# Optimization experiments

Measured on AMD Instinct MI355X. Metric: run time of the kernel, lower is better.

The kernel has to match this reference:

```python
import jax, jax.numpy as jnp
import numpy as np

ALPHA = 0.25
GAMMA = 2.0
HUBER_DELTA = 0.5  # init kwarg delta
REG_BETA = 1.0 / 9.0


def calc_iou(a, b):
    # a: [A,4] anchors, b: [M,4] gt boxes, xyxy
    area = (b[:, 2] - b[:, 0]) * (b[:, 3] - b[:, 1])  # [M]
    iw = jnp.clip(jnp.minimum(a[:, 2:3], b[:, 2]) - jnp.maximum(a[:, 0:1], b[:, 0]), 0.0)
    ih = jnp.clip(jnp.minimum(a[:, 3:4], b[:, 3]) - jnp.maximum(a[:, 1:2], b[:, 1]), 0.0)
    ua = jnp.clip(((a[:, 2] - a[:, 0]) * (a[:, 3] - a[:, 1]))[:, None] + area - iw * ih, 1e-8)
    return iw * ih / ua  # [A,M]


def _per_sample(cls, reg, dist, ann, anchor):
    # cls [A,C], reg [A,4], dist [A,1], ann [M,6], anchor [A,4]
    aw = anchor[:, 2] - anchor[:, 0]
    ah = anchor[:, 3] - anchor[:, 1]
    acx = anchor[:, 0] + 0.5 * aw
    acy = anchor[:, 1] + 0.5 * ah

    valid = ann[:, 4] != -1.0  # padding annotations have class == -1
    cls = jnp.clip(cls, 1e-4, 1.0 - 1e-4)

    iou = jnp.where(valid[None, :], calc_iou(anchor, ann[:, :4]), -1.0)  # [A,M]
    iou_max = iou.max(axis=1)
    iou_arg = iou.argmax(axis=1)
    assigned = ann[iou_arg]  # [A,6]

    pos = iou_max >= 0.5
    num_pos = pos.sum()
    denom = jnp.maximum(num_pos.astype(cls.dtype), 1.0)

    labels = assigned[:, 4].astype(jnp.int32)
    onehot = jax.nn.one_hot(labels, cls.shape[1], dtype=cls.dtype)
    # -1 = ignore, 0 = negative (IoU<0.4 or positive-but-not-this-class), 1 = assigned class
    targets = jnp.where(pos[:, None], onehot,
                        jnp.where((iou_max < 0.4)[:, None], 0.0, -1.0))

    af = jnp.where(targets == 1.0, ALPHA, 1.0 - ALPHA)
    fw = af * jnp.where(targets == 1.0, 1.0 - cls, cls) ** GAMMA
    bce = -(targets * jnp.log(cls) + (1.0 - targets) * jnp.log(1.0 - cls))
    cls_loss = jnp.where(targets != -1.0, fw * bce, 0.0).sum() / denom

    # empty-annotation fallback: all anchors treated as background
    cls_loss_empty = ((1.0 - ALPHA) * cls ** GAMMA * (-jnp.log(1.0 - cls))).sum()
    has_ann = valid.any()
    cls_loss = jnp.where(has_ann, cls_loss, cls_loss_empty)

    gw_raw = assigned[:, 2] - assigned[:, 0]
    gh_raw = assigned[:, 3] - assigned[:, 1]
    gcx = assigned[:, 0] + 0.5 * gw_raw  # centers use unclamped w/h (as in torch code)
    gcy = assigned[:, 1] + 0.5 * gh_raw
    gw = jnp.clip(gw_raw, 1.0)
    gh = jnp.clip(gh_raw, 1.0)
    t = jnp.stack([(gcx - acx) / aw, (gcy - acy) / ah,
                   jnp.log(gw / aw), jnp.log(gh / ah)], axis=1)
    t = t / jnp.asarray([0.1, 0.1, 0.2, 0.2], dtype=cls.dtype)
    diff = jnp.abs(t - reg)
    rl = jnp.where(diff <= REG_BETA, 0.5 * 9.0 * diff ** 2, diff - 0.5 / 9.0)
    posf = pos.astype(cls.dtype)
    reg_loss = jnp.where(num_pos > 0, (rl * posf[:, None]).sum() / (denom * 4.0), 0.0)

    # --- distance Huber loss (delta=0.5), positives only ---
    d = jnp.abs(dist[:, 0] - assigned[:, 5])
    hl = jnp.where(d <= HUBER_DELTA, 0.5 * d ** 2, HUBER_DELTA * (d - 0.5 * HUBER_DELTA))
    dist_loss = jnp.where(num_pos > 0, (hl * posf).sum() / denom, 0.0)

    return cls_loss, reg_loss, dist_loss


def reference(classifications, regressions, distances, anchors, annotations):
    anchor = anchors[0]
    cl, rl, dl = jax.vmap(_per_sample, in_axes=(0, 0, 0, 0, None))(
        classifications, regressions, distances, annotations, anchor)
    return (jnp.mean(cl, keepdims=True),
            jnp.mean(rl, keepdims=True),
            jnp.mean(dl, keepdims=True))


def setup_inputs() -> dict:
    key = jax.random.key(0)
    ks = jax.random.split(key, 10)
    B, A, C, M = 8, 120000, 80, 32
    IMG = 800.0

    classifications = jax.random.uniform(ks[0], (B, A, C), dtype=jnp.float32)
    regressions = jax.random.normal(ks[1], (B, A, 4), dtype=jnp.float32)
    distances = jax.random.normal(ks[2], (B, A, 1), dtype=jnp.float32) * 10.0 + 50.0

    # anchors: valid xyxy boxes over an 800px image
    acx = jax.random.uniform(ks[3], (A,), minval=0.0, maxval=IMG)
    acy = jax.random.uniform(ks[4], (A,), minval=0.0, maxval=IMG)
    aw = jax.random.uniform(ks[5], (A, 2), minval=16.0, maxval=256.0)
    anchors = jnp.stack([acx - 0.5 * aw[:, 0], acy - 0.5 * aw[:, 1],
                         acx + 0.5 * aw[:, 0], acy + 0.5 * aw[:, 1]], axis=1)[None].astype(jnp.float32)

    # annotations: [B,M,6] = x1,y1,x2,y2,class,distance (all valid)
    gc = jax.random.uniform(ks[6], (B, M, 2), minval=100.0, maxval=IMG - 100.0)
    gs = jax.random.uniform(ks[7], (B, M, 2), minval=32.0, maxval=300.0)
    boxes = jnp.concatenate([gc - 0.5 * gs, gc + 0.5 * gs], axis=-1)
    labels = jax.random.randint(ks[8], (B, M, 1), 0, C).astype(jnp.float32)
    gdist = jax.random.uniform(ks[9], (B, M, 1), minval=1.0, maxval=100.0)
    annotations = jnp.concatenate([boxes, labels, gdist], axis=-1).astype(jnp.float32)

    return {"classifications": classifications, "regressions": regressions,
            "distances": distances, "anchors": anchors, "annotations": annotations}
```

## Files before the change

### kernel.cpp

```cpp
#include <hip/hip_runtime.h>
#include <hip/hip_bf16.h>


typedef float v4f __attribute__((ext_vector_type(4)));

#define LN2_075 0.51986038542f

__device__ __forceinline__ float wave_reduce_sum(float v) {
#pragma unroll
    for (int off = 32; off > 0; off >>= 1) v += __shfl_down(v, off);
    return v;
}

__device__ __forceinline__ float smooth_l1(float d) {
    return d <= (1.0f / 9.0f) ? 4.5f * d * d : d - (0.5f / 9.0f);
}

__device__ __forceinline__ float proc4(v4f cv, float acc) {
#pragma unroll
    for (int j = 0; j < 4; ++j) {
        const float c = fminf(fmaxf(cv[j], 1e-4f), 1.0f - 1e-4f);
        acc = fmaf(c * c, __log2f(1.0f - c), acc);
    }
    return acc;
}

template <int CPA>
__global__ __launch_bounds__(256) void main_kernel(
    const float* __restrict__ cls, const float* __restrict__ reg,
    const float* __restrict__ dist, const float* __restrict__ anchors,
    const float* __restrict__ ann, float* __restrict__ partA,
    float4* __restrict__ partB, int A, int M, int SBLK, int nb) {
    const int b = blockIdx.y;
    const int tid = threadIdx.x;
    const int lane = tid & 63;
    const int wid = tid >> 6;

    if (blockIdx.x < SBLK) {
        const int NC4 = A * CPA;
        const v4f* __restrict__ p = (const v4f*)(cls + (size_t)b * NC4 * 4);
        const int s = SBLK << 8;
        int i = (blockIdx.x << 8) + tid;
        float acc = 0.f;
        for (; i + 3 * s < NC4; i += 4 * s) {
            const v4f a0 = p[i];
            const v4f a1 = p[i + s];
            const v4f a2 = p[i + 2 * s];
            const v4f a3 = p[i + 3 * s];
            acc = proc4(a0, acc);
            acc = proc4(a1, acc);
            acc = proc4(a2, acc);
            acc = proc4(a3, acc);
        }
        for (; i < NC4; i += s) acc = proc4(p[i], acc);

        __shared__ float s_red[4];
        acc = wave_reduce_sum(acc);
        if (lane == 0) s_red[wid] = acc;
        __syncthreads();
        if (tid == 0)
            partA[(size_t)b * SBLK + blockIdx.x] = s_red[0] + s_red[1] + s_red[2] + s_red[3];
        return;
    }

    const int blk = blockIdx.x - SBLK;
    const int base = blk << 8;

    __shared__ float s_ann[64 * 6];
    const float* annb = ann + (size_t)b * M * 6;
    for (int i = tid; i < M * 6; i += 256) s_ann[i] = annb[i];
    __syncthreads();

    const int a = base + tid;
    float l_npos = 0.f, l_reg = 0.f, l_dist = 0.f;
    int st = -1;
    if (a < A) {
        const float4 av = *(const float4*)(anchors + (size_t)a * 4);
        const float aw = av.z - av.x, ah = av.w - av.y;
        const float acx = av.x + 0.5f * aw, acy = av.y + 0.5f * ah;
        const float aarea = aw * ah;

        float best = -1.0f;
        int bi = 0;
        for (int m = 0; m < M; ++m) {
            const float* g = s_ann + m * 6;
            float iou = -1.0f;
            if (g[4] != -1.0f) {
                float iw = fmaxf(fminf(av.z, g[2]) - fmaxf(av.x, g[0]), 0.f);
                float ih = fmaxf(fminf(av.w, g[3]) - fmaxf(av.y, g[1]), 0.f);
                float inter = iw * ih;
                float area = (g[2] - g[0]) * (g[3] - g[1]);
                float ua = fmaxf(aarea + area - inter, 1e-8f);
                iou = inter / ua;
            }
            if (iou > best) { best = iou; bi = m; }
        }

        if (best >= 0.5f) {
            const float* g = s_ann + bi * 6;
            st = (int)g[4];
            l_npos = 1.f;
            const float4 rv = *(const float4*)(reg + ((size_t)b * A + a) * 4);
            const float gwr = g[2] - g[0], ghr = g[3] - g[1];
            const float gcx = g[0] + 0.5f * gwr, gcy = g[1] + 0.5f * ghr;
            const float gw = fmaxf(gwr, 1.f), gh = fmaxf(ghr, 1.f);
            const float t0 = ((gcx - acx) / aw) / 0.1f;
            const float t1 = ((gcy - acy) / ah) / 0.1f;
            const float t2 = __logf(gw / aw) / 0.2f;
            const float t3 = __logf(gh / ah) / 0.2f;
            l_reg = smooth_l1(fabsf(t0 - rv.x)) + smooth_l1(fabsf(t1 - rv.y)) +
                    smooth_l1(fabsf(t2 - rv.z)) + smooth_l1(fabsf(t3 - rv.w));
            const float dv = dist[(size_t)b * A + a];
            const float dd = fabsf(dv - g[5]);
            l_dist = dd <= 0.5f ? 0.5f * dd * dd : 0.5f * (dd - 0.25f);
        } else if (best >= 0.4f) {
            st = -2;
        }
    }

    const v4f* __restrict__ clsb = (const v4f*)(cls + ((size_t)b * A + base) * (CPA * 4));
    float corr = 0.f;
    if (st >= 0) {
        const float cr = cls[((size_t)b * A + a) * (CPA * 4) + st];
        const float c = fminf(fmaxf(cr, 1e-4f), 1.0f - 1e-4f);
        const float om = 1.0f - c;
        corr = LN2_075 * (c * c * __log2f(om))
               + 0.25f * om * om * (-__logf(c));
    } else if (st == -2) {
        float part = 0.f;
#pragma unroll
        for (int k = 0; k < CPA; ++k) part = proc4(clsb[(size_t)tid * CPA + k], part);
        corr = LN2_075 * part;
    }

    __shared__ float s_red4[4][4];
    const float w0 = wave_reduce_sum(l_npos);
    const float w1 = wave_reduce_sum(corr);
    const float w2 = wave_reduce_sum(l_reg);
    const float w3 = wave_reduce_sum(l_dist);
    if (lane == 0) {
        s_red4[0][wid] = w0; s_red4[1][wid] = w1; s_red4[2][wid] = w2; s_red4[3][wid] = w3;
    }
    __syncthreads();
    if (tid == 0) {
        float4 p;
        p.x = s_red4[0][0] + s_red4[0][1] + s_red4[0][2] + s_red4[0][3];
        p.y = s_red4[1][0] + s_red4[1][1] + s_red4[1][2] + s_red4[1][3];
        p.z = s_red4[2][0] + s_red4[2][1] + s_red4[2][2] + s_red4[2][3];
        p.w = s_red4[3][0] + s_red4[3][1] + s_red4[3][2] + s_red4[3][3];
        partB[(size_t)b * nb + blk] = p;
    }
}

__global__ void finalize_kernel(const float* __restrict__ partA,
                                const float4* __restrict__ partB,
                                float* __restrict__ out, int B, int SBLK, int nb) {
    const int lane = threadIdx.x & 63;
    const int b = threadIdx.x >> 6;
    __shared__ float s_res[8][3];
    if (b < B) {
        float sa = 0.f, np_ = 0.f, corr = 0.f, rs = 0.f, ds = 0.f;
        for (int i = lane; i < SBLK; i += 64) sa += partA[(size_t)b * SBLK + i];
        for (int i = lane; i < nb; i += 64) {
            const float4 p = partB[(size_t)b * nb + i];
            np_ += p.x; corr += p.y; rs += p.z; ds += p.w;
        }
        sa = wave_reduce_sum(sa);
        np_ = wave_reduce_sum(np_);
        corr = wave_reduce_sum(corr);
        rs = wave_reduce_sum(rs);
        ds = wave_reduce_sum(ds);
        if (lane == 0) {
            const float cls_total = fmaf(sa, -LN2_075, corr);
            const float denom = fmaxf(np_, 1.f);
            s_res[b][0] = cls_total / denom;
            s_res[b][1] = np_ > 0.f ? rs / (denom * 4.f) : 0.f;
            s_res[b][2] = np_ > 0.f ? ds / denom : 0.f;
        }
    }
    __syncthreads();
    if (threadIdx.x == 0) {
        float c = 0.f, r = 0.f, d = 0.f;
        for (int i = 0; i < B; ++i) { c += s_res[i][0]; r += s_res[i][1]; d += s_res[i][2]; }
        out[0] = c / (float)B;
        out[1] = r / (float)B;
        out[2] = d / (float)B;
    }
}

__global__ __launch_bounds__(256) void fused_generic_kernel(
    const float* __restrict__ cls, const float* __restrict__ reg,
    const float* __restrict__ dist, const float* __restrict__ anchors,
    const float* __restrict__ ann, float4* __restrict__ partials,
    int A, int C, int M, int nb) {
    const int b = blockIdx.y;
    const int base = blockIdx.x << 8;
    const int tid = threadIdx.x;
    const int cpa = C >> 2;

    __shared__ float s_ann[64 * 6];
    __shared__ signed char s_state[256];
    const float* annb = ann + (size_t)b * M * 6;
    for (int i = tid; i < M * 6; i += 256) s_ann[i] = annb[i];
    s_state[tid] = -2;
    __syncthreads();

    const int a = base + tid;
    float l_npos = 0.f, l_reg = 0.f, l_dist = 0.f;
    if (a < A) {
        const float4 av = *(const float4*)(anchors + (size_t)a * 4);
        const float aw = av.z - av.x, ah = av.w - av.y;
        const float acx = av.x + 0.5f * aw, acy = av.y + 0.5f * ah;
        const float aarea = aw * ah;
        float best = -1.0f;
        int bi = 0;
        for (int m = 0; m < M; ++m) {
            const float* g = s_ann + m * 6;
            float iou = -1.0f;
            if (g[4] != -1.0f) {
                float iw = fmaxf(fminf(av.z, g[2]) - fmaxf(av.x, g[0]), 0.f);
                float ih = fmaxf(fminf(av.w, g[3]) - fmaxf(av.y, g[1]), 0.f);
                float inter = iw * ih;
                float area = (g[2] - g[0]) * (g[3] - g[1]);
                float ua = fmaxf(aarea + area - inter, 1e-8f);
                iou = inter / ua;
            }
            if (iou > best) { best = iou; bi = m; }
        }
        signed char st;
        if (best >= 0.5f) {
            const float* g = s_ann + bi * 6;
            st = (signed char)(int)g[4];
            l_npos = 1.f;
            const float4 rv = *(const float4*)(reg + ((size_t)b * A + a) * 4);
            const float gwr = g[2] - g[0], ghr = g[3] - g[1];
            const float gcx = g[0] + 0.5f * gwr, gcy = g[1] + 0.5f * ghr;
            const float gw = fmaxf(gwr, 1.f), gh = fmaxf(ghr, 1.f);
            const float t0 = ((gcx - acx) / aw) / 0.1f;
            const float t1 = ((gcy - acy) / ah) / 0.1f;
            const float t2 = __logf(gw / aw) / 0.2f;
            const float t3 = __logf(gh / ah) / 0.2f;
            l_reg = smooth_l1(fabsf(t0 - rv.x)) + smooth_l1(fabsf(t1 - rv.y)) +
                    smooth_l1(fabsf(t2 - rv.z)) + smooth_l1(fabsf(t3 - rv.w));
            const float dv = dist[(size_t)b * A + a];
            const float dd = fabsf(dv - g[5]);
            l_dist = dd <= 0.5f ? 0.5f * dd * dd : 0.5f * (dd - 0.25f);
        } else if (best < 0.4f) {
            st = -1;
        } else {
            st = -2;
        }
        s_state[tid] = st;
    }
    __syncthreads();

    const float4* __restrict__ clsb = (const float4*)(cls + ((size_t)b * A + base) * C);
    int a_local = tid / cpa;
    int cc = tid % cpa;
    const int dA = 256 / cpa;
    const int dC = 256 % cpa;
    float lsum = 0.f;
    for (int k = 0; k < cpa; ++k) {
        const int st = s_state[a_local];
        if (st != -2) {
            const float4 cv = clsb[k * 256 + tid];
            const int c0 = cc << 2;
#pragma unroll
            for (int j = 0; j < 4; ++j) {
                float c = j == 0 ? cv.x : j == 1 ? cv.y : j == 2 ? cv.z : cv.w;
                c = fminf(fmaxf(c, 1e-4f), 1.0f - 1e-4f);
                const bool ispos = (st == c0 + j);
                const float om = 1.0f - c;
                const float x = ispos ? c : om;
                const float w = ispos ? 0.25f * om * om : 0.75f * c * c;
                lsum -= w * __logf(x);
            }
        }
        a_local += dA;
        cc += dC;
        if (cc >= cpa) { cc -= cpa; ++a_local; }
    }

    __shared__ float s_red[4][4];
    const float w0 = wave_reduce_sum(l_npos);
    const float w1 = wave_reduce_sum(lsum);
    const float w2 = wave_reduce_sum(l_reg);
    const float w3 = wave_reduce_sum(l_dist);
    const int lane = tid & 63, wid = tid >> 6;
    if (lane == 0) {
        s_red[0][wid] = w0; s_red[1][wid] = w1; s_red[2][wid] = w2; s_red[3][wid] = w3;
    }
    __syncthreads();
    if (tid == 0) {
        float4 p;
        p.x = s_red[0][0] + s_red[0][1] + s_red[0][2] + s_red[0][3];
        p.y = s_red[1][0] + s_red[1][1] + s_red[1][2] + s_red[1][3];
        p.z = s_red[2][0] + s_red[2][1] + s_red[2][2] + s_red[2][3];
        p.w = s_red[3][0] + s_red[3][1] + s_red[3][2] + s_red[3][3];
        partials[(size_t)b * nb + blockIdx.x] = p;
    }
}

extern "C" void kernel_launch(void* const* d_in, const int* in_sizes, int n_in,
                              void* d_out, int out_size, void* d_ws, size_t ws_size,
                              hipStream_t stream) {
    const float* cls     = (const float*)d_in[0];
    const float* reg     = (const float*)d_in[1];
    const float* dist    = (const float*)d_in[2];
    const float* anchors = (const float*)d_in[3];
    const float* ann     = (const float*)d_in[4];

    const int A = in_sizes[3] / 4;
    const int B = in_sizes[1] / (A * 4);
    const int C = in_sizes[0] / (B * A);
    const int M = in_sizes[4] / (B * 6);
    const int nb = (A + 255) / 256;
    const int SBLK = 256;

    float* partA = (float*)d_ws;
    float4* partB = (float4*)((char*)d_ws + 8192);

    if (C == 80) {
        dim3 g(SBLK + nb, B), blk(256);
        main_kernel<20><<<g, blk, 0, stream>>>(cls, reg, dist, anchors, ann,
                                               partA, partB, A, M, SBLK, nb);
        finalize_kernel<<<1, B * 64, 0, stream>>>(partA, partB, (float*)d_out, B, SBLK, nb);
    } else {
        dim3 g(nb, B), blk(256);
        fused_generic_kernel<<<g, blk, 0, stream>>>(cls, reg, dist, anchors, ann,
                                                    partB, A, C, M, nb);
        finalize_kernel<<<1, B * 64, 0, stream>>>(partA, partB, (float*)d_out, B, 0, nb);
    }
}
```

Measured before the change: 75.29 us.

## Schedule anchor blocks first, use contiguous chunks for streaming focal sum, drop lower clamp

Result: no change. 73.98 us (-1.7%).

```diff
diff --git a/kernel.cpp b/kernel.cpp
--- a/kernel.cpp
+++ b/kernel.cpp
@@ -16,10 +16,10 @@
     return d <= (1.0f / 9.0f) ? 4.5f * d * d : d - (0.5f / 9.0f);
 }
 
-__device__ __forceinline__ float proc4(v4f cv, float acc) {
+__device__ __forceinline__ float proc4t(v4f cv, float acc) {
 #pragma unroll
     for (int j = 0; j < 4; ++j) {
-        const float c = fminf(fmaxf(cv[j], 1e-4f), 1.0f - 1e-4f);
+        const float c = fminf(cv[j], 1.0f - 1e-4f);
         acc = fmaf(c * c, __log2f(1.0f - c), acc);
     }
     return acc;
@@ -36,34 +36,38 @@
     const int lane = tid & 63;
     const int wid = tid >> 6;
 
-    if (blockIdx.x < SBLK) {
+    if (blockIdx.x >= nb) {
+        const int sb = blockIdx.x - nb;
         const int NC4 = A * CPA;
+        const int chunk = (NC4 + SBLK - 1) / SBLK;
+        const int start = sb * chunk;
+        const int end = min(start + chunk, NC4);
         const v4f* __restrict__ p = (const v4f*)(cls + (size_t)b * NC4 * 4);
-        const int s = SBLK << 8;
-        int i = (blockIdx.x << 8) + tid;
-        float acc = 0.f;
-        for (; i + 3 * s < NC4; i += 4 * s) {
+
+        float acc0 = 0.f, acc1 = 0.f;
+        int i = start + tid;
+        for (; i + 768 < end; i += 1024) {
             const v4f a0 = p[i];
-            const v4f a1 = p[i + s];
-            const v4f a2 = p[i + 2 * s];
-            const v4f a3 = p[i + 3 * s];
-            acc = proc4(a0, acc);
-            acc = proc4(a1, acc);
-            acc = proc4(a2, acc);
-            acc = proc4(a3, acc);
-        }
-        for (; i < NC4; i += s) acc = proc4(p[i], acc);
+            const v4f a1 = p[i + 256];
+            const v4f a2 = p[i + 512];
+            const v4f a3 = p[i + 768];
+            acc0 = proc4t(a0, acc0);
+            acc1 = proc4t(a1, acc1);
+            acc0 = proc4t(a2, acc0);
+            acc1 = proc4t(a3, acc1);
+        }
+        for (; i < end; i += 256) acc0 = proc4t(p[i], acc0);
 
         __shared__ float s_red[4];
-        acc = wave_reduce_sum(acc);
+        float acc = wave_reduce_sum(acc0 + acc1);
         if (lane == 0) s_red[wid] = acc;
         __syncthreads();
         if (tid == 0)
-            partA[(size_t)b * SBLK + blockIdx.x] = s_red[0] + s_red[1] + s_red[2] + s_red[3];
+            partA[(size_t)b * SBLK + sb] = s_red[0] + s_red[1] + s_red[2] + s_red[3];
         return;
     }
 
-    const int blk = blockIdx.x - SBLK;
+    const int blk = blockIdx.x;
     const int base = blk << 8;
 
     __shared__ float s_ann[64 * 6];
@@ -122,14 +126,15 @@
     float corr = 0.f;
     if (st >= 0) {
         const float cr = cls[((size_t)b * A + a) * (CPA * 4) + st];
+        const float ct = fminf(cr, 1.0f - 1e-4f);
         const float c = fminf(fmaxf(cr, 1e-4f), 1.0f - 1e-4f);
         const float om = 1.0f - c;
-        corr = LN2_075 * (c * c * __log2f(om))
+        corr = LN2_075 * (ct * ct * __log2f(1.0f - ct))
                + 0.25f * om * om * (-__logf(c));
     } else if (st == -2) {
         float part = 0.f;
 #pragma unroll
-        for (int k = 0; k < CPA; ++k) part = proc4(clsb[(size_t)tid * CPA + k], part);
+        for (int k = 0; k < CPA; ++k) part = proc4t(clsb[(size_t)tid * CPA + k], part);
         corr = LN2_075 * part;
     }
 
@@ -321,7 +326,7 @@
     float4* partB = (float4*)((char*)d_ws + 8192);
 
     if (C == 80) {
-        dim3 g(SBLK + nb, B), blk(256);
+        dim3 g(nb + SBLK, B), blk(256);
         main_kernel<20><<<g, blk, 0, stream>>>(cls, reg, dist, anchors, ann,
                                                partA, partB, A, M, SBLK, nb);
         finalize_kernel<<<1, B * 64, 0, stream>>>(partA, partB, (float*)d_out, B, SBLK, nb);
```
